# Kernel tuning notes

Measured on AMD Instinct MI355X. Metric: run time of the kernel, lower is better.

The kernel has to match this reference:

```python
import jax, jax.numpy as jnp
import numpy as np

# --- geometry constants (ProtoDUNE-HD-like) ---
B, F, T = 1, 1, 256            # batch, input features, nticks
NCHANS = 2560                   # total readout channels (800+800+480+480)
NWIRES = [800, 800, 480]        # wires per plane (U, V, W) on each face
NCELLS = 40000                  # number of 3-wire crossing cells per face
MLP_HID, MLP_OUT = 8, 2

# channel ranges per (face, plane): induction planes (U,V) wrap both faces,
# collection (W) channels are disjoint per face
_CHAN_RANGES = {(0, 0): (0, 800), (0, 1): (800, 1600), (0, 2): (1600, 2080),
                (1, 0): (0, 800), (1, 1): (800, 1600), (1, 2): (2080, 2560)}


def _make_tables():
    rng = np.random.default_rng(0)
    wcs = {}
    for (f, p), (lo, hi) in _CHAN_RANGES.items():
        n = hi - lo
        ch = lo + rng.permutation(n)                       # irregular wire->channel map
        wcs[(f, p)] = np.stack([np.arange(n), ch], axis=1).astype(np.int64)
    gi = {}
    for f in (0, 1):
        gi[f] = np.stack([rng.integers(0, NWIRES[p], NCELLS) for p in range(3)],
                         axis=1).astype(np.int64)          # (NCELLS, 3) wire idx per plane
    return wcs, gi


def setup_inputs() -> dict:
    key = jax.random.key(0)
    k = jax.random.split(key, 5)
    wcs, gi = _make_tables()
    inp = {
        'x':  jax.random.normal(k[0], (B, F, NCHANS, T), jnp.float32),
        'W1': jax.random.normal(k[1], (3 * F, MLP_HID), jnp.float32) * 0.5,
        'b1': jax.random.normal(k[2], (MLP_HID,), jnp.float32) * 0.1,
        'W2': jax.random.normal(k[3], (MLP_HID, MLP_OUT), jnp.float32) * 0.5,
        'b2': jax.random.normal(k[4], (MLP_OUT,), jnp.float32) * 0.1,
        'gi0': jnp.asarray(gi[0]), 'gi1': jnp.asarray(gi[1]),
    }
    for f in (0, 1):
        for p in range(3):
            inp[f'wc{f}{p}'] = jnp.asarray(wcs[(f, p)])
    return inp


def _make_wires(x, wc):
    # wires[..., wire_ident, :] = x[..., channel, :]   (Network.make_wires)
    Bb, Ff, _, Tt = x.shape
    wires = jnp.zeros((Bb, Ff, wc.shape[0], Tt), x.dtype)
    return wires.at[:, :, wc[:, 0], :].set(x[:, :, wc[:, 1], :])


def _crossview_mlp(x, W1, b1, W2, b2, wcs, gis):
    # mp_step: relu -> per-face cross-view gather -> MLP -> amax scatter -> concat
    x = jax.nn.relu(x)
    Bb, Ff, C, Tt = x.shape
    scattered = jnp.zeros((Bb, MLP_OUT, C, Tt), x.dtype)   # zeros init => amax includes 0
    for f in range(2):
        gi = gis[f]
        # gather the three plane views for each crossing cell: (B, 3F, NCELLS, T)
        cells = jnp.concatenate(
            [_make_wires(x, wcs[f][p])[:, :, gi[:, p], :] for p in range(3)], axis=1)
        h = jnp.einsum('bfnt,fh->bhnt', cells, W1) + b1[None, :, None, None]
        y = jnp.einsum('bhnt,ho->bont', h, W2) + b2[None, :, None, None]
        # scatter_to_chans: amax-reduce cell outputs back onto readout channels
        for p in range(3):
            ch = wcs[f][p][gi[:, p], 1]                    # channel of each cell's wire
            scattered = scattered.at[:, :, ch, :].max(y)
    # special_style == 'mlp': concat input features with cross-view MLP features
    return jnp.concatenate([x, scattered], axis=1)         # (B, F+MLP_OUT, C, T)


def reference(x, W1, b1, W2, b2, wc00, wc01, wc02, wc10, wc11, wc12, gi0, gi1):
    wcs = ((wc00, wc01, wc02), (wc10, wc11, wc12))
    gis = (gi0, gi1)
    return _crossview_mlp(x, W1, b1, W2, b2, wcs, gis)
```

## Files before the change

kernel.cpp:

```cpp
#include <hip/hip_runtime.h>

#define NCHANS 2560
#define TT 256
#define NCELLS_ 40000
#define NFC (2 * NCELLS_)
#define CAP 192
#define NCHUNK (CAP / 64)

#define WS_CURSOR 0
#define WS_XR     16384
#define WS_EPACK  1327104

#define PREP_BLOCKS 640
#define FILL_BLOCKS 313

__device__ __forceinline__ unsigned int bf16rne(float f) {
    unsigned int b = __float_as_uint(f);
    return (b + 0x7FFFu + ((b >> 16) & 1u)) >> 16;
}

__global__ __launch_bounds__(256) void prep_fill_kernel(
    const float* __restrict__ x,
    const int* __restrict__ gi0, const int* __restrict__ gi1,
    const int* __restrict__ wc00, const int* __restrict__ wc01, const int* __restrict__ wc02,
    const int* __restrict__ wc10, const int* __restrict__ wc11, const int* __restrict__ wc12,
    int* __restrict__ cursor, uint2* __restrict__ epack, uint2* __restrict__ xr,
    float* __restrict__ out)
{
    const int b = blockIdx.x;
    if (b < PREP_BLOCKS) {
        const int i = b * 256 + threadIdx.x;
        float4 v = ((const float4*)x)[i];
        v.x = fmaxf(v.x, 0.f); v.y = fmaxf(v.y, 0.f);
        v.z = fmaxf(v.z, 0.f); v.w = fmaxf(v.w, 0.f);
        ((float4*)out)[i] = v;
        uint2 p;
        p.x = bf16rne(v.x) | (bf16rne(v.y) << 16);
        p.y = bf16rne(v.z) | (bf16rne(v.w) << 16);
        xr[i] = p;
    } else {
        const int i = (b - PREP_BLOCKS) * 256 + threadIdx.x;
        if (i >= NFC) return;
        const int face = (i >= NCELLS_) ? 1 : 0;
        const int cell = i - face * NCELLS_;
        const int* gi = face ? gi1 : gi0;
        const int w0 = gi[cell * 3 + 0];
        const int w1 = gi[cell * 3 + 1];
        const int w2 = gi[cell * 3 + 2];
        const int* wcA = face ? wc10 : wc00;
        const int* wcB = face ? wc11 : wc01;
        const int* wcC = face ? wc12 : wc02;
        const int c0 = wcA[w0 * 2 + 1];
        const int c1 = wcB[w1 * 2 + 1];
        const int c2 = wcC[w2 * 2 + 1];
        uint2 E;
        E.x = (unsigned)c0 | ((unsigned)c1 << 16);
        E.y = (unsigned)c2;
        int s;
        s = atomicAdd(&cursor[c0], 1); if (s < CAP) epack[c0 * CAP + s] = E;
        s = atomicAdd(&cursor[c1], 1); if (s < CAP) epack[c1 * CAP + s] = E;
        s = atomicAdd(&cursor[c2], 1); if (s < CAP) epack[c2 * CAP + s] = E;
    }
}

__global__ __launch_bounds__(256) void gather_kernel(
    const float* __restrict__ W1, const float* __restrict__ b1,
    const float* __restrict__ W2, const float* __restrict__ b2,
    const int* __restrict__ cursor, const uint2* __restrict__ epack,
    const char* __restrict__ xr, float* __restrict__ out)
{
    float A[3][2], C[2];
#pragma unroll
    for (int o = 0; o < 2; ++o) {
        float s = b2[o];
#pragma unroll
        for (int h = 0; h < 8; ++h) s += b1[h] * W2[h * 2 + o];
        C[o] = s;
    }
#pragma unroll
    for (int p = 0; p < 3; ++p)
#pragma unroll
        for (int o = 0; o < 2; ++o) {
            float s = 0.f;
#pragma unroll
            for (int h = 0; h < 8; ++h) s += W1[p * 8 + h] * W2[h * 2 + o];
            A[p][o] = s;
        }

    __shared__ uint2 sE[4][64];
    const int w = threadIdx.x >> 6;
    const int lane = threadIdx.x & 63;
    const int ch = blockIdx.x * 2 + (w >> 1);
    const int half = w & 1;
    const int t0 = half * 128 + lane * 2;
    const int byteoff = t0 * 2;

    const int n = min(cursor[ch], CAP);
    const uint2* ep = epack + ch * CAP;

    float m00 = 0.f, m01 = 0.f, m10 = 0.f, m11 = 0.f;

    for (int cb = 0; cb < NCHUNK; ++cb) {
        const int base = cb * 64;
        int k = n - base; k = k < 0 ? 0 : (k > 64 ? 64 : k);
        if (lane < k) sE[w][lane] = ep[base + lane];
        __syncthreads();
#pragma unroll 2
        for (int e = 0; e < k; ++e) {
            const uint2 E = sE[w][e];
            const int c0 = E.x & 0xFFFFu;
            const int c1 = E.x >> 16;
            const int c2 = E.y;
            const unsigned int d0 = *(const unsigned int*)(xr + (c0 << 9) + byteoff);
            const unsigned int d1 = *(const unsigned int*)(xr + (c1 << 9) + byteoff);
            const unsigned int d2 = *(const unsigned int*)(xr + (c2 << 9) + byteoff);
            const float f0a = __uint_as_float(d0 << 16), f0b = __uint_as_float(d0 & 0xFFFF0000u);
            const float f1a = __uint_as_float(d1 << 16), f1b = __uint_as_float(d1 & 0xFFFF0000u);
            const float f2a = __uint_as_float(d2 << 16), f2b = __uint_as_float(d2 & 0xFFFF0000u);
            const float ya0 = fmaf(A[0][0], f0a, fmaf(A[1][0], f1a, fmaf(A[2][0], f2a, C[0])));
            const float yb0 = fmaf(A[0][0], f0b, fmaf(A[1][0], f1b, fmaf(A[2][0], f2b, C[0])));
            const float ya1 = fmaf(A[0][1], f0a, fmaf(A[1][1], f1a, fmaf(A[2][1], f2a, C[1])));
            const float yb1 = fmaf(A[0][1], f0b, fmaf(A[1][1], f1b, fmaf(A[2][1], f2b, C[1])));
            m00 = fmaxf(m00, ya0); m01 = fmaxf(m01, yb0);
            m10 = fmaxf(m10, ya1); m11 = fmaxf(m11, yb1);
        }
        __syncthreads();
    }

    float2* o1 = (float2*)(out + NCHANS * TT + ch * TT + t0);
    float2* o2 = (float2*)(out + 2 * NCHANS * TT + ch * TT + t0);
    *o1 = make_float2(m00, m01);
    *o2 = make_float2(m10, m11);
}

extern "C" void kernel_launch(void* const* d_in, const int* in_sizes, int n_in,
                              void* d_out, int out_size, void* d_ws, size_t ws_size,
                              hipStream_t stream) {
    const float* x  = (const float*)d_in[0];
    const float* W1 = (const float*)d_in[1];
    const float* b1 = (const float*)d_in[2];
    const float* W2 = (const float*)d_in[3];
    const float* b2 = (const float*)d_in[4];
    const int* gi0  = (const int*)d_in[5];
    const int* gi1  = (const int*)d_in[6];
    const int* wc00 = (const int*)d_in[7];
    const int* wc01 = (const int*)d_in[8];
    const int* wc02 = (const int*)d_in[9];
    const int* wc10 = (const int*)d_in[10];
    const int* wc11 = (const int*)d_in[11];
    const int* wc12 = (const int*)d_in[12];
    float* out = (float*)d_out;

    char* ws = (char*)d_ws;
    int*   cursor = (int*)(ws + WS_CURSOR);
    uint2* xr     = (uint2*)(ws + WS_XR);
    uint2* epack  = (uint2*)(ws + WS_EPACK);

    hipMemsetAsync(cursor, 0, NCHANS * sizeof(int), stream);

    prep_fill_kernel<<<PREP_BLOCKS + FILL_BLOCKS, 256, 0, stream>>>(
        x, gi0, gi1, wc00, wc01, wc02, wc10, wc11, wc12,
        cursor, epack, xr, out);

    gather_kernel<<<NCHANS / 2, 256, 0, stream>>>(
        W1, b1, W2, b2, cursor, epack, (const char*)xr, out);
}
```

Before: 77.27 us.

## Switch gather math to packed fp16, drop LDS staging, one atomic per instance

Stores the relu'd input copy as fp16 instead of bf16 and runs the folded MLP with packed half2 FMA and v_pk_max_f16 instead of scalar fp32 math. The gather loop now reads edge entries straight from global memory with a wave-uniform channel, so the shared-memory staging and block barriers are gone. The fill stage launches one thread per (cell, plane) instance, each doing a single atomic, which spreads the atomics over more threads. Doing the accumulation in fp16 loses precision and can overflow for large values.

```diff
diff --git a/kernel.cpp b/kernel.cpp
--- a/kernel.cpp
+++ b/kernel.cpp
@@ -1,22 +1,26 @@
 #include <hip/hip_runtime.h>
+#include <hip/hip_fp16.h>
 
 #define NCHANS 2560
 #define TT 256
 #define NCELLS_ 40000
-#define NFC (2 * NCELLS_)
+#define NINST 240000
+#define HALF_NINST 120000
 #define CAP 192
-#define NCHUNK (CAP / 64)
 
 #define WS_CURSOR 0
 #define WS_XR     16384
 #define WS_EPACK  1327104
 
 #define PREP_BLOCKS 640
-#define FILL_BLOCKS 313
+#define FILL_BLOCKS 938
 
-__device__ __forceinline__ unsigned int bf16rne(float f) {
-    unsigned int b = __float_as_uint(f);
-    return (b + 0x7FFFu + ((b >> 16) & 1u)) >> 16;
+__device__ __forceinline__ __half2 pk_max_f16(__half2 a, __half2 b) {
+    unsigned int ua = *(unsigned int*)&a;
+    unsigned int ub = *(unsigned int*)&b;
+    unsigned int ur;
+    asm("v_pk_max_f16 %0, %1, %2" : "=v"(ur) : "v"(ua), "v"(ub));
+    return *(__half2*)&ur;
 }
 
 __global__ __launch_bounds__(256) void prep_fill_kernel(
@@ -34,32 +38,35 @@
         v.x = fmaxf(v.x, 0.f); v.y = fmaxf(v.y, 0.f);
         v.z = fmaxf(v.z, 0.f); v.w = fmaxf(v.w, 0.f);
         ((float4*)out)[i] = v;
+        __half2 h01 = __floats2half2_rn(v.x, v.y);
+        __half2 h23 = __floats2half2_rn(v.z, v.w);
         uint2 p;
-        p.x = bf16rne(v.x) | (bf16rne(v.y) << 16);
-        p.y = bf16rne(v.z) | (bf16rne(v.w) << 16);
+        p.x = *(unsigned int*)&h01;
+        p.y = *(unsigned int*)&h23;
         xr[i] = p;
     } else {
-        const int i = (b - PREP_BLOCKS) * 256 + threadIdx.x;
-        if (i >= NFC) return;
-        const int face = (i >= NCELLS_) ? 1 : 0;
-        const int cell = i - face * NCELLS_;
+        const int j = (b - PREP_BLOCKS) * 256 + threadIdx.x;
+        if (j >= NINST) return;
+        const int face = (j >= HALF_NINST) ? 1 : 0;
+        const int i = j - face * HALF_NINST;
+        const int p = i % 3;
+        const int cellBase = i - p;
         const int* gi = face ? gi1 : gi0;
-        const int w0 = gi[cell * 3 + 0];
-        const int w1 = gi[cell * 3 + 1];
-        const int w2 = gi[cell * 3 + 2];
+        const int w0 = gi[cellBase + 0];
+        const int w1 = gi[cellBase + 1];
+        const int w2 = gi[cellBase + 2];
         const int* wcA = face ? wc10 : wc00;
         const int* wcB = face ? wc11 : wc01;
         const int* wcC = face ? wc12 : wc02;
         const int c0 = wcA[w0 * 2 + 1];
         const int c1 = wcB[w1 * 2 + 1];
         const int c2 = wcC[w2 * 2 + 1];
+        const int cOwn = (p == 0) ? c0 : ((p == 1) ? c1 : c2);
         uint2 E;
         E.x = (unsigned)c0 | ((unsigned)c1 << 16);
         E.y = (unsigned)c2;
-        int s;
-        s = atomicAdd(&cursor[c0], 1); if (s < CAP) epack[c0 * CAP + s] = E;
-        s = atomicAdd(&cursor[c1], 1); if (s < CAP) epack[c1 * CAP + s] = E;
-        s = atomicAdd(&cursor[c2], 1); if (s < CAP) epack[c2 * CAP + s] = E;
+        const int s = atomicAdd(&cursor[cOwn], 1);
+        if (s < CAP) epack[cOwn * CAP + s] = E;
     }
 }
 
@@ -86,51 +93,49 @@
             for (int h = 0; h < 8; ++h) s += W1[p * 8 + h] * W2[h * 2 + o];
             A[p][o] = s;
         }
+    __half2 a2[3][2], C2[2];
+#pragma unroll
+    for (int p = 0; p < 3; ++p)
+#pragma unroll
+        for (int o = 0; o < 2; ++o) a2[p][o] = __half2half2(__float2half(A[p][o]));
+    C2[0] = __half2half2(__float2half(C[0]));
+    C2[1] = __half2half2(__float2half(C[1]));
 
-    __shared__ uint2 sE[4][64];
     const int w = threadIdx.x >> 6;
     const int lane = threadIdx.x & 63;
-    const int ch = blockIdx.x * 2 + (w >> 1);
-    const int half = w & 1;
-    const int t0 = half * 128 + lane * 2;
-    const int byteoff = t0 * 2;
+    const int wid = blockIdx.x * 4 + w;
+    int ch = wid >> 1;
+    const int half = wid & 1;
+    ch = __builtin_amdgcn_readfirstlane(ch);
 
-    const int n = min(cursor[ch], CAP);
+    int n = cursor[ch];
+    n = n < CAP ? n : CAP;
     const uint2* ep = epack + ch * CAP;
+    const char* base = xr + half * 256 + lane * 4;
 
-    float m00 = 0.f, m01 = 0.f, m10 = 0.f, m11 = 0.f;
+    __half2 m0 = __half2half2(__float2half(0.f));
+    __half2 m1 = m0;
 
-    for (int cb = 0; cb < NCHUNK; ++cb) {
-        const int base = cb * 64;
-        int k = n - base; k = k < 0 ? 0 : (k > 64 ? 64 : k);
-        if (lane < k) sE[w][lane] = ep[base + lane];
-        __syncthreads();
 #pragma unroll 2
-        for (int e = 0; e < k; ++e) {
-            const uint2 E = sE[w][e];
-            const int c0 = E.x & 0xFFFFu;
-            const int c1 = E.x >> 16;
-            const int c2 = E.y;
-            const unsigned int d0 = *(const unsigned int*)(xr + (c0 << 9) + byteoff);
-            const unsigned int d1 = *(const unsigned int*)(xr + (c1 << 9) + byteoff);
-            const unsigned int d2 = *(const unsigned int*)(xr + (c2 << 9) + byteoff);
-            const float f0a = __uint_as_float(d0 << 16), f0b = __uint_as_float(d0 & 0xFFFF0000u);
-            const float f1a = __uint_as_float(d1 << 16), f1b = __uint_as_float(d1 & 0xFFFF0000u);
-            const float f2a = __uint_as_float(d2 << 16), f2b = __uint_as_float(d2 & 0xFFFF0000u);
-            const float ya0 = fmaf(A[0][0], f0a, fmaf(A[1][0], f1a, fmaf(A[2][0], f2a, C[0])));
-            const float yb0 = fmaf(A[0][0], f0b, fmaf(A[1][0], f1b, fmaf(A[2][0], f2b, C[0])));
-            const float ya1 = fmaf(A[0][1], f0a, fmaf(A[1][1], f1a, fmaf(A[2][1], f2a, C[1])));
-            const float yb1 = fmaf(A[0][1], f0b, fmaf(A[1][1], f1b, fmaf(A[2][1], f2b, C[1])));
-            m00 = fmaxf(m00, ya0); m01 = fmaxf(m01, yb0);
-            m10 = fmaxf(m10, ya1); m11 = fmaxf(m11, yb1);
-        }
-        __syncthreads();
+    for (int e = 0; e < n; ++e) {
+        const uint2 E = ep[e];
+        const int c0 = E.x & 0xFFFFu;
+        const int c1 = E.x >> 16;
+        const int c2 = E.y;
+        const __half2 f0 = *(const __half2*)(base + (c0 << 9));
+        const __half2 f1 = *(const __half2*)(base + (c1 << 9));
+        const __half2 f2 = *(const __half2*)(base + (c2 << 9));
+        const __half2 y0 = __hfma2(a2[0][0], f0, __hfma2(a2[1][0], f1, __hfma2(a2[2][0], f2, C2[0])));
+        const __half2 y1 = __hfma2(a2[0][1], f0, __hfma2(a2[1][1], f1, __hfma2(a2[2][1], f2, C2[1])));
+        m0 = pk_max_f16(m0, y0);
+        m1 = pk_max_f16(m1, y1);
     }
 
-    float2* o1 = (float2*)(out + NCHANS * TT + ch * TT + t0);
-    float2* o2 = (float2*)(out + 2 * NCHANS * TT + ch * TT + t0);
-    *o1 = make_float2(m00, m01);
-    *o2 = make_float2(m10, m11);
+    const int off = ch * TT + half * 128 + lane * 2;
+    float2* o1 = (float2*)(out + NCHANS * TT + off);
+    float2* o2 = (float2*)(out + 2 * NCHANS * TT + off);
+    *o1 = make_float2(__low2float(m0), __high2float(m0));
+    *o2 = make_float2(__low2float(m1), __high2float(m1));
 }
 
 extern "C" void kernel_launch(void* const* d_in, const int* in_sizes, int n_in,
@@ -156,12 +161,12 @@
     uint2* xr     = (uint2*)(ws + WS_XR);
     uint2* epack  = (uint2*)(ws + WS_EPACK);
 
-    hipMemsetAsync(cursor, 0, NCHANS * sizeof(int), stream);
+    (void)hipMemsetAsync(cursor, 0, NCHANS * sizeof(int), stream);
 
     prep_fill_kernel<<<PREP_BLOCKS + FILL_BLOCKS, 256, 0, stream>>>(
         x, gi0, gi1, wc00, wc01, wc02, wc10, wc11, wc12,
         cursor, epack, xr, out);
 
-    gather_kernel<<<NCHANS / 2, 256, 0, stream>>>(
+    gather_kernel<<<NCHANS * 2 / 4, 256, 0, stream>>>(
         W1, b1, W2, b2, cursor, epack, (const char*)xr, out);
 }
```

New measurement: 76.74 us. No clear change (-0.7%).
